# Optimization experiments

Measured on AMD Instinct MI355X. Metric: run time of the kernel, lower is better.

## Reference

```python
import jax, jax.numpy as jnp
import numpy as np

D_MODEL, D_STATE, D_CONV, D_INNER = 1024, 16, 4, 2048
BATCH, SEQ = 4, 2048


def silu(v):
    return v * jax.nn.sigmoid(v)


def setup_inputs() -> dict:
    key = jax.random.key(0)
    ks = jax.random.split(key, 7)
    x = jax.random.normal(ks[0], (BATCH, SEQ, D_MODEL), dtype=jnp.float32)
    s = 0.02
    W_in = jax.random.normal(ks[1], (D_MODEL, 2 * D_INNER), dtype=jnp.float32) * s
    conv_w = jax.random.normal(ks[2], (D_INNER, 1, D_CONV), dtype=jnp.float32) * s  # depthwise (O, I/g=1, K)
    conv_b = jax.random.normal(ks[3], (D_INNER,), dtype=jnp.float32) * s
    W_xproj = jax.random.normal(ks[4], (D_INNER, 2 * D_STATE + 1), dtype=jnp.float32) * s
    A_log = jnp.log(jnp.tile(jnp.arange(1, D_STATE + 1, dtype=jnp.float32), (D_INNER, 1)))
    D = jnp.ones((D_INNER,), dtype=jnp.float32)
    W_out = jax.random.normal(ks[5], (D_INNER, D_MODEL), dtype=jnp.float32) * s
    return {"x": x, "W_in": W_in, "conv_w": conv_w, "conv_b": conv_b,
            "W_xproj": W_xproj, "A_log": A_log, "D": D, "W_out": W_out}


def reference(x, W_in, conv_w, conv_b, W_xproj, A_log, D, W_out):
    B, L, _ = x.shape
    xz = x @ W_in                                   # (B, L, 2*d_inner)
    x_proj, z = jnp.split(xz, 2, axis=-1)
    # Depthwise causal conv: padding=d_conv-1 then truncate to L == left-pad only.
    xc = jax.lax.conv_general_dilated(
        x_proj.transpose(0, 2, 1), conv_w,
        window_strides=(1,), padding=[(D_CONV - 1, 0)],
        feature_group_count=D_INNER,
        dimension_numbers=("NCH", "OIH", "NCH"))
    x_conv = silu((xc + conv_b[None, :, None]).transpose(0, 2, 1))  # (B, L, d_inner)
    ssm = x_conv @ W_xproj                           # (B, L, 1+2*d_state)
    delta = jax.nn.softplus(ssm[..., 0])             # (B, L)
    Bm = ssm[..., 1:1 + D_STATE]                     # (B, L, d_state)
    Cm = ssm[..., 1 + D_STATE:]                      # (B, L, d_state)
    # Original: deltaA = exp(delta*A) and softmax weights are computed but unused.
    deltaB = delta[..., None] * Bm                   # (B, L, d_state)
    # h_approx = mean_L(x outer deltaB): avoid (B,L,d_inner,d_state) intermediate.
    h_mean = jnp.einsum("bld,bln->bdn", x_conv, deltaB) / L  # (B, d_inner, d_state)
    y = jnp.einsum("bdn,bln->bld", h_mean, Cm)       # (B, L, d_inner)
    y = y + D[None, None, :] * x_conv
    y = y * silu(z)
    return y @ W_out                                 # (B, L, d_model)
```

## Files before the change

### kernel.cpp

```cpp
#include <hip/hip_runtime.h>
#include <hip/hip_bf16.h>
#include <stdint.h>

typedef __bf16 bf16x8 __attribute__((ext_vector_type(8)));
typedef float f32x4 __attribute__((ext_vector_type(4)));
typedef float f32x2 __attribute__((ext_vector_type(2)));
typedef unsigned short u16;
typedef u16 ushort4v __attribute__((ext_vector_type(4)));
typedef u16 ushort8v __attribute__((ext_vector_type(8)));

__device__ __forceinline__ u16 f2bf(float f) {
    union { float f; uint32_t u; } v; v.f = f;
    uint32_t u = v.u + 0x7FFFu + ((v.u >> 16) & 1u);
    return (u16)(u >> 16);
}
__device__ __forceinline__ float bf2f(u16 b) {
    union { uint32_t u; float f; } v; v.u = ((uint32_t)b) << 16;
    return v.f;
}
__device__ __forceinline__ float silu_f(float v) {
    return v / (1.0f + __expf(-v));
}
__device__ __forceinline__ void gload_lds16(const u16* g, u16* l) {
    __builtin_amdgcn_global_load_lds(
        (const __attribute__((address_space(1))) void*)g,
        (__attribute__((address_space(3))) void*)l, 16, 0, 0);
}

__device__ __forceinline__ void trans_tile(
        const float* __restrict__ src, u16* __restrict__ dst, int R, int C,
        int bc, int br, float (*tt)[33], int tid) {
    const int tx = tid & 31, ty = tid >> 5;
#pragma unroll
    for (int i = 0; i < 4; i++)
        tt[ty + i * 8][tx] = src[(int64_t)(br * 32 + ty + i * 8) * C + bc * 32 + tx];
    __syncthreads();
#pragma unroll
    for (int i = 0; i < 4; i++)
        dst[(int64_t)(bc * 32 + ty + i * 8) * R + br * 32 + tx] = f2bf(tt[tx][ty + i * 8]);
}

__global__ __launch_bounds__(256) void prep_k(
        const float* __restrict__ x, u16* __restrict__ x_bf,
        const float* __restrict__ Wi, u16* __restrict__ Wti,
        const float* __restrict__ Wo, u16* __restrict__ Wto,
        const float* __restrict__ wx, u16* __restrict__ wxt) {
    __shared__ float tt[32][33];
    const int blk = blockIdx.x, tid = threadIdx.x;
    if (blk < 8192) {
        int i = blk * 256 + tid;
        float4 v = *(const float4*)&x[(int64_t)i * 4];
        ushort4v o = { f2bf(v.x), f2bf(v.y), f2bf(v.z), f2bf(v.w) };
        *(ushort4v*)&x_bf[(int64_t)i * 4] = o;
    } else if (blk < 12288) {
        int t = blk - 8192;
        trans_tile(Wi, Wti, 1024, 4096, t & 127, t >> 7, tt, tid);
    } else if (blk < 14336) {
        int t = blk - 12288;
        trans_tile(Wo, Wto, 2048, 1024, t & 31, t >> 5, tt, tid);
    } else {
        int idx = (blk - 14336) * 256 + tid;
        int j = idx >> 11, d = idx & 2047;
        wxt[idx] = (j < 33) ? f2bf(wx[d * 33 + j]) : (u16)0;
    }
}

template<int M_REP, int WARPS_M, int B_HALVES, bool OUT_BF16>
__global__ __launch_bounds__(512) void gemm_dp(
        const u16* __restrict__ A, const u16* __restrict__ Bt,
        void* __restrict__ Cout, int nbn_sh, int NT, int lda, int ldb, int ldc) {
    constexpr int WARPS_N = 8 / WARPS_M;
    constexpr int QPT = M_REP / 2;
    constexpr int WV_M = M_REP * 16;
    constexpr int BN = WARPS_N * 64;
    constexpr int B_T = BN * 64;

    __shared__ __align__(16) u16 As[2 * 16384];
    __shared__ __align__(16) u16 Bs[2 * B_T];

    const int tid = threadIdx.x;
    const int wave = tid >> 6;
    const int lane = tid & 63;
    const int wm = wave / WARPS_N, wn = wave % WARPS_N;
    const int fr = lane & 15, fq = lane >> 4;

    const int nwg = gridDim.x;
    const int cpx = nwg >> 3;
    const int swz = (blockIdx.x & 7) * cpx + (blockIdx.x >> 3);
    const int bm = swz >> nbn_sh;
    const int bn = swz & ((1 << nbn_sh) - 1);

    const int srow = tid >> 3;
    const int scol8 = ((tid & 7) ^ (srow & 7)) * 8;
    const u16* gA = A + (int64_t)(bm * 256 + srow) * lda + scol8;
    const u16* gB = Bt + (int64_t)(bn * BN + srow) * ldb + scol8;
    const int64_t lda64 = lda, ldb64 = ldb;

    const int ksw0 = ((fq) ^ (fr & 7)) * 8;
    const int ksw1 = ((4 + fq) ^ (fr & 7)) * 8;
    const int arow0 = (wm * WV_M + fr) * 64;
    const int brow0 = (wn * 64 + fr) * 64;

    auto STAGE_A_HALF = [&](int kt, int buf, int h) {
#pragma unroll
        for (int j = 0; j < 2; ++j)
            gload_lds16(gA + (int64_t)(h * 128 + j * 64) * lda64 + kt * 64,
                        &As[buf * 16384 + h * 8192 + j * 4096 + tid * 8]);
    };
    auto STAGE_B_HALF = [&](int kt, int buf, int h) {
#pragma unroll
        for (int j = 0; j < 2; ++j)
            gload_lds16(gB + (int64_t)(h * 128 + j * 64) * ldb64 + kt * 64,
                        &Bs[buf * B_T + h * 8192 + j * 4096 + tid * 8]);
    };

    f32x4 acc[M_REP][4] = {};

    STAGE_A_HALF(0, 0, 0); STAGE_A_HALF(0, 0, 1);
#pragma unroll
    for (int h = 0; h < B_HALVES; ++h) STAGE_B_HALF(0, 0, h);
#pragma unroll
    for (int h = 0; h < B_HALVES; ++h) STAGE_B_HALF(1, 1, h);
    if constexpr (B_HALVES == 2) { asm volatile("s_waitcnt vmcnt(4)" ::: "memory"); }
    else                         { asm volatile("s_waitcnt vmcnt(2)" ::: "memory"); }
    __builtin_amdgcn_s_barrier();

    const int NI = NT >> 1;
    for (int s = 0; s < NI; ++s) {
        const bool more = (s + 1 < NI);
#pragma unroll
        for (int t = 0; t < 2; ++t) {
            const u16* Ab = &As[t * 16384];
            const u16* Bb = &Bs[t * B_T];
            bf16x8 breg[4][2];
            bf16x8 areg[2][2][2];
#pragma unroll
            for (int q = 0; q < QPT; ++q) {
                const int p = q & 1;
                if (q == 0) {
#pragma unroll
                    for (int n = 0; n < 4; ++n) {
                        breg[n][0] = *(const bf16x8*)(Bb + brow0 + n * 1024 + ksw0);
                        breg[n][1] = *(const bf16x8*)(Bb + brow0 + n * 1024 + ksw1);
                    }
#pragma unroll
                    for (int j = 0; j < 2; ++j) {
                        areg[0][j][0] = *(const bf16x8*)(Ab + arow0 + j * 1024 + ksw0);
                        areg[0][j][1] = *(const bf16x8*)(Ab + arow0 + j * 1024 + ksw1);
                    }
                }
                __builtin_amdgcn_s_setprio(1);
                if (q + 1 < QPT) {
#pragma unroll
                    for (int j = 0; j < 2; ++j) {
                        areg[p ^ 1][j][0] = *(const bf16x8*)(Ab + arow0 + (2 * (q + 1) + j) * 1024 + ksw0);
                        areg[p ^ 1][j][1] = *(const bf16x8*)(Ab + arow0 + (2 * (q + 1) + j) * 1024 + ksw1);
                    }
                }
#pragma unroll
                for (int j = 0; j < 2; ++j)
#pragma unroll
                    for (int n = 0; n < 4; ++n) {
                        acc[2 * q + j][n] = __builtin_amdgcn_mfma_f32_16x16x32_bf16(
                            areg[p][j][0], breg[n][0], acc[2 * q + j][n], 0, 0, 0);
                        acc[2 * q + j][n] = __builtin_amdgcn_mfma_f32_16x16x32_bf16(
                            areg[p][j][1], breg[n][1], acc[2 * q + j][n], 0, 0, 0);
                    }
                if (q + 1 < QPT) {
#pragma unroll
                    for (int g = 0; g < 4; ++g) {
                        __builtin_amdgcn_sched_group_barrier(0x008, 2, 0);
                        __builtin_amdgcn_sched_group_barrier(0x100, 1, 0);
                        __builtin_amdgcn_sched_group_barrier(0x008, 2, 0);
                    }
                }
                __builtin_amdgcn_s_setprio(0);
                if constexpr (QPT == 4) {
                    if (t == 0 && q == 0)         STAGE_A_HALF(2 * s + 1, 1, 0);
                    if (t == 0 && q == 1)         STAGE_A_HALF(2 * s + 1, 1, 1);
                    if (t == 0 && q == 2 && more) STAGE_B_HALF(2 * s + 2, 0, 0);
                    if (t == 0 && q == 3 && more) STAGE_B_HALF(2 * s + 2, 0, 1);
                    if (t == 1 && q == 0 && more) STAGE_A_HALF(2 * s + 2, 0, 0);
                    if (t == 1 && q == 1 && more) STAGE_A_HALF(2 * s + 2, 0, 1);
                    if (t == 1 && q == 2 && more) STAGE_B_HALF(2 * s + 3, 1, 0);
                    if (t == 1 && q == 3 && more) STAGE_B_HALF(2 * s + 3, 1, 1);
                } else {
                    if (t == 0 && q == 0)         STAGE_A_HALF(2 * s + 1, 1, 0);
                    if (t == 0 && q == 1) {       STAGE_A_HALF(2 * s + 1, 1, 1);
                        if (more)                 STAGE_B_HALF(2 * s + 2, 0, 0); }
                    if (t == 1 && q == 0 && more) STAGE_A_HALF(2 * s + 2, 0, 0);
                    if (t == 1 && q == 1 && more) { STAGE_A_HALF(2 * s + 2, 0, 1);
                                                    STAGE_B_HALF(2 * s + 3, 1, 0); }
                }
                if (q == QPT - 1) {
                    if (more) {
                        if constexpr (B_HALVES == 2) { asm volatile("s_waitcnt vmcnt(4)" ::: "memory"); }
                        else                         { asm volatile("s_waitcnt vmcnt(2)" ::: "memory"); }
                    } else {
                        asm volatile("s_waitcnt vmcnt(0)" ::: "memory");
                    }
                }
                __builtin_amdgcn_s_barrier();
            }
        }
    }

#pragma unroll
    for (int m = 0; m < M_REP; ++m) {
#pragma unroll
        for (int n = 0; n < 4; ++n) {
            const int col = bn * BN + wn * 64 + n * 16 + fr;
#pragma unroll
            for (int r = 0; r < 4; ++r) {
                const int row = bm * 256 + wm * WV_M + m * 16 + fq * 4 + r;
                if constexpr (OUT_BF16)
                    ((u16*)Cout)[(int64_t)row * ldc + col] = f2bf(acc[m][n][r]);
                else
                    ((float*)Cout)[(int64_t)row * ldc + col] = acc[m][n][r];
            }
        }
    }
}

__global__ __launch_bounds__(256) void conv_ssm_k(
        const u16* __restrict__ xz, const float* __restrict__ cw,
        const float* __restrict__ cb, const u16* __restrict__ wxt,
        u16* __restrict__ xc, float* __restrict__ dB, float* __restrict__ Cm) {
    __shared__ __align__(16) u16 Xs[16][2064];
    __shared__ float Sred[4][16][48];
    __shared__ float deltas[16];
    const int blk = blockIdx.x;
    const int b = blk >> 7, lb = blk & 127;
    const int l0 = lb << 4;
    const int64_t r0 = (int64_t)b * 2048 + l0;
    const int tid = threadIdx.x;
    const int d0 = tid * 8;

    float w[8][4], bias[8];
#pragma unroll
    for (int j = 0; j < 8; j++) {
        float4 wv = *(const float4*)&cw[(d0 + j) * 4];
        w[j][0] = wv.x; w[j][1] = wv.y; w[j][2] = wv.z; w[j][3] = wv.w;
        bias[j] = cb[d0 + j];
    }
    float win[4][8];
#pragma unroll
    for (int r = 0; r < 3; r++) {
        int l = l0 - 3 + r;
        if (l < 0) {
#pragma unroll
            for (int j = 0; j < 8; j++) win[r][j] = 0.f;
        } else {
            ushort8v v = *(const ushort8v*)&xz[((int64_t)b * 2048 + l) * 4096 + d0];
#pragma unroll
            for (int j = 0; j < 8; j++) win[r][j] = bf2f(v[j]);
        }
    }
#pragma unroll
    for (int li = 0; li < 16; li++) {
        ushort8v v = *(const ushort8v*)&xz[(r0 + li) * 4096 + d0];
#pragma unroll
        for (int j = 0; j < 8; j++) win[(3 + li) & 3][j] = bf2f(v[j]);
        ushort8v o;
#pragma unroll
        for (int j = 0; j < 8; j++) {
            float s = bias[j];
#pragma unroll
            for (int k = 0; k < 4; k++) s += w[j][k] * win[(li + k) & 3][j];
            o[j] = f2bf(silu_f(s));
        }
        *(ushort8v*)&xc[(r0 + li) * 2048 + d0] = o;
        *(ushort8v*)&Xs[li][d0] = o;
    }
    __syncthreads();

    const int kc = tid >> 6;
    const int lane = tid & 63;
    const int fr = lane & 15, fq = lane >> 4;
    const u16* bp = wxt + (int64_t)fr * 2048 + kc * 512 + fq * 8;
    const u16* ap = &Xs[fr][kc * 512 + fq * 8];
    f32x4 acc0 = {}, acc1 = {}, acc2 = {};
#pragma unroll 4
    for (int k = 0; k < 512; k += 32) {
        bf16x8 av = *(const bf16x8*)(ap + k);
        bf16x8 b0 = *(const bf16x8*)(bp + k);
        bf16x8 b1 = *(const bf16x8*)(bp + 16 * 2048 + k);
        bf16x8 b2 = *(const bf16x8*)(bp + 32 * 2048 + k);
        acc0 = __builtin_amdgcn_mfma_f32_16x16x32_bf16(av, b0, acc0, 0, 0, 0);
        acc1 = __builtin_amdgcn_mfma_f32_16x16x32_bf16(av, b1, acc1, 0, 0, 0);
        acc2 = __builtin_amdgcn_mfma_f32_16x16x32_bf16(av, b2, acc2, 0, 0, 0);
    }
#pragma unroll
    for (int r = 0; r < 4; r++) {
        Sred[kc][fq * 4 + r][fr]      = acc0[r];
        Sred[kc][fq * 4 + r][16 + fr] = acc1[r];
        Sred[kc][fq * 4 + r][32 + fr] = acc2[r];
    }
    __syncthreads();
    if (tid < 16) {
        float s0 = Sred[0][tid][0] + Sred[1][tid][0] + Sred[2][tid][0] + Sred[3][tid][0];
        deltas[tid] = (s0 > 20.f) ? s0 : log1pf(__expf(s0));
    }
    __syncthreads();
    {
        const int row = tid >> 4, n = tid & 15;
        float sB = Sred[0][row][1 + n] + Sred[1][row][1 + n] +
                   Sred[2][row][1 + n] + Sred[3][row][1 + n];
        float sC = Sred[0][row][17 + n] + Sred[1][row][17 + n] +
                   Sred[2][row][17 + n] + Sred[3][row][17 + n];
        dB[(r0 + row) * 16 + n] = deltas[row] * sB * (1.0f / 2048.0f);
        Cm[(r0 + row) * 16 + n] = sC;
    }
}

__global__ __launch_bounds__(256) void h_part_k(
        const u16* __restrict__ xc, const float* __restrict__ dB,
        float* __restrict__ hp) {
    const int blk = blockIdx.x;
    const int dt = blk & 7, b = (blk >> 3) & 3, lc = blk >> 5;
    const int d = dt * 256 + threadIdx.x;
    const u16* xp = xc + ((int64_t)(b * 2048 + lc * 64)) * 2048 + d;
    const f32x2* dbp = (const f32x2*)(dB + (int64_t)(b * 2048 + lc * 64) * 16);
    f32x2 acc[8] = {};
    for (int l = 0; l < 64; l++) {
        float xv = bf2f(xp[(int64_t)l * 2048]);
#pragma unroll
        for (int q = 0; q < 8; q++) acc[q] += dbp[l * 8 + q] * xv;
    }
    float* o = hp + ((int64_t)((lc * 4 + b) * 2048 + d)) * 16;
#pragma unroll
    for (int q = 0; q < 8; q++) *(f32x2*)&o[q * 2] = acc[q];
}

__global__ void h_red_k(const float* __restrict__ hp, float* __restrict__ h) {
    const int i = blockIdx.x * 256 + threadIdx.x;
    float s = 0.f;
#pragma unroll
    for (int c = 0; c < 32; c++) s += hp[(int64_t)c * 131072 + i];
    h[i] = s;
}

__global__ __launch_bounds__(256) void y_gate_k(
        u16* __restrict__ xz, const u16* __restrict__ xc,
        const float* __restrict__ h, const float* __restrict__ Cm,
        const float* __restrict__ Dp) {
    const int blk = blockIdx.x;
    const int lc = blk & 63, dt = (blk >> 6) & 1, b = blk >> 7;
    const int d0 = dt * 1024 + threadIdx.x * 4;
    const float* hpp = h + ((int64_t)(b * 2048 + d0)) * 16;
    float hreg[4][16];
#pragma unroll
    for (int i = 0; i < 4; i++)
#pragma unroll
        for (int n = 0; n < 16; n++) hreg[i][n] = hpp[i * 16 + n];
    float Dv[4];
#pragma unroll
    for (int i = 0; i < 4; i++) Dv[i] = Dp[d0 + i];
    __shared__ float Cs[32][16];
    if (threadIdx.x < 128)
        ((float4*)&Cs[0][0])[threadIdx.x] =
            ((const float4*)(Cm + (int64_t)(b * 2048 + lc * 32) * 16))[threadIdx.x];
    __syncthreads();
    for (int li = 0; li < 32; li++) {
        const int64_t rowz = (int64_t)(b * 2048 + lc * 32 + li);
        ushort4v xcv = *(const ushort4v*)&xc[rowz * 2048 + d0];
        ushort4v zv = *(const ushort4v*)&xz[rowz * 4096 + 2048 + d0];
        ushort4v o;
#pragma unroll
        for (int i = 0; i < 4; i++) {
            float s = Dv[i] * bf2f(xcv[i]);
#pragma unroll
            for (int n = 0; n < 16; n++) s += hreg[i][n] * Cs[li][n];
            o[i] = f2bf(s * silu_f(bf2f(zv[i])));
        }
        *(ushort4v*)&xz[rowz * 4096 + d0] = o;
    }
}

extern "C" void kernel_launch(void* const* d_in, const int* in_sizes, int n_in,
                              void* d_out, int out_size, void* d_ws, size_t ws_size,
                              hipStream_t stream) {
    (void)in_sizes; (void)n_in; (void)out_size; (void)ws_size;
    const float* x      = (const float*)d_in[0];
    const float* W_in   = (const float*)d_in[1];
    const float* conv_w = (const float*)d_in[2];
    const float* conv_b = (const float*)d_in[3];
    const float* W_xp   = (const float*)d_in[4];
    const float* Dp     = (const float*)d_in[6];
    const float* W_out  = (const float*)d_in[7];
    float* out = (float*)d_out;
    char* ws = (char*)d_ws;

    u16*   x_bf   = (u16*)(ws);
    float* dB     = (float*)(ws);
    float* Cm     = (float*)(ws + 524288);
    float* h      = (float*)(ws + 1048576);
    float* hp     = (float*)(ws + 1572864);
    u16*   Wt_in  = (u16*)(ws + 16777216);
    u16*   Wt_out = (u16*)(ws + 25165824);
    u16*   Wxt    = (u16*)(ws + 29360128);
    u16*   xz     = (u16*)(ws + 29556736);
    u16*   xcv    = (u16*)(ws + 96665600);

    prep_k<<<14720, 256, 0, stream>>>(x, x_bf, W_in, Wt_in, W_out, Wt_out, W_xp, Wxt);
    gemm_dp<8, 2, 2, true><<<512, 512, 0, stream>>>(x_bf, Wt_in, xz, 4, 16, 1024, 1024, 4096);
    conv_ssm_k<<<512, 256, 0, stream>>>(xz, conv_w, conv_b, Wxt, xcv, dB, Cm);
    h_part_k<<<1024, 256, 0, stream>>>(xcv, dB, hp);
    h_red_k<<<512, 256, 0, stream>>>(hp, h);
    y_gate_k<<<512, 256, 0, stream>>>(xz, xcv, h, Cm, Dp);
    gemm_dp<4, 4, 1, false><<<256, 512, 0, stream>>>(xz, Wt_out, out, 3, 32, 4096, 2048, 1024);
}
```

Before: 209.8 us.

## Triple-buffer A tiles in GEMM and lengthen h_part chunks to cut reduction

The GEMM's A operand moves from double to triple buffering in LDS, with rotating slot indices. This lets A for tile k+2 be prefetched while tiles k and k+1 are consumed, and the vmcnt waits are raised to allow more loads in flight. Separately, h_part_k now processes 256-row chunks instead of 64, so it launches 4x fewer blocks and h_red_k sums 8 partials instead of 32. The trade-offs are more LDS per GEMM block (possibly lower occupancy) and less parallelism in h_part_k.

New measurement: 223.3 us. 6.4% more time.

```diff
diff --git a/kernel.cpp b/kernel.cpp
--- a/kernel.cpp
+++ b/kernel.cpp
@@ -75,7 +75,7 @@
     constexpr int BN = WARPS_N * 64;
     constexpr int B_T = BN * 64;
 
-    __shared__ __align__(16) u16 As[2 * 16384];
+    __shared__ __align__(16) u16 As[3 * 16384];
     __shared__ __align__(16) u16 Bs[2 * B_T];
 
     const int tid = threadIdx.x;
@@ -101,11 +101,11 @@
     const int arow0 = (wm * WV_M + fr) * 64;
     const int brow0 = (wn * 64 + fr) * 64;
 
-    auto STAGE_A_HALF = [&](int kt, int buf, int h) {
+    auto STAGE_A_HALF = [&](int kt, int slot, int h) {
 #pragma unroll
         for (int j = 0; j < 2; ++j)
             gload_lds16(gA + (int64_t)(h * 128 + j * 64) * lda64 + kt * 64,
-                        &As[buf * 16384 + h * 8192 + j * 4096 + tid * 8]);
+                        &As[slot * 16384 + h * 8192 + j * 4096 + tid * 8]);
     };
     auto STAGE_B_HALF = [&](int kt, int buf, int h) {
 #pragma unroll
@@ -119,18 +119,21 @@
     STAGE_A_HALF(0, 0, 0); STAGE_A_HALF(0, 0, 1);
 #pragma unroll
     for (int h = 0; h < B_HALVES; ++h) STAGE_B_HALF(0, 0, h);
+    STAGE_A_HALF(1, 1, 0); STAGE_A_HALF(1, 1, 1);
 #pragma unroll
     for (int h = 0; h < B_HALVES; ++h) STAGE_B_HALF(1, 1, h);
-    if constexpr (B_HALVES == 2) { asm volatile("s_waitcnt vmcnt(4)" ::: "memory"); }
-    else                         { asm volatile("s_waitcnt vmcnt(2)" ::: "memory"); }
+    if constexpr (B_HALVES == 2) { asm volatile("s_waitcnt vmcnt(8)" ::: "memory"); }
+    else                         { asm volatile("s_waitcnt vmcnt(6)" ::: "memory"); }
     __builtin_amdgcn_s_barrier();
 
+    int a0 = 0, a1 = 1, a2 = 2;
     const int NI = NT >> 1;
     for (int s = 0; s < NI; ++s) {
         const bool more = (s + 1 < NI);
 #pragma unroll
         for (int t = 0; t < 2; ++t) {
-            const u16* Ab = &As[t * 16384];
+            const int aslot = (t == 0) ? a0 : a1;
+            const u16* Ab = &As[aslot * 16384];
             const u16* Bb = &Bs[t * B_T];
             bf16x8 breg[4][2];
             bf16x8 areg[2][2][2];
@@ -175,27 +178,22 @@
                     }
                 }
                 __builtin_amdgcn_s_setprio(0);
+                const int ktn = 2 * s + 2 + t;
+                const int asl = (t == 0) ? a2 : a0;
                 if constexpr (QPT == 4) {
-                    if (t == 0 && q == 0)         STAGE_A_HALF(2 * s + 1, 1, 0);
-                    if (t == 0 && q == 1)         STAGE_A_HALF(2 * s + 1, 1, 1);
-                    if (t == 0 && q == 2 && more) STAGE_B_HALF(2 * s + 2, 0, 0);
-                    if (t == 0 && q == 3 && more) STAGE_B_HALF(2 * s + 2, 0, 1);
-                    if (t == 1 && q == 0 && more) STAGE_A_HALF(2 * s + 2, 0, 0);
-                    if (t == 1 && q == 1 && more) STAGE_A_HALF(2 * s + 2, 0, 1);
-                    if (t == 1 && q == 2 && more) STAGE_B_HALF(2 * s + 3, 1, 0);
-                    if (t == 1 && q == 3 && more) STAGE_B_HALF(2 * s + 3, 1, 1);
+                    if (q == 0 && more) STAGE_A_HALF(ktn, asl, 0);
+                    if (q == 1 && more) STAGE_A_HALF(ktn, asl, 1);
+                    if (q == 2 && more) STAGE_B_HALF(ktn, t, 0);
+                    if (q == 3 && more) STAGE_B_HALF(ktn, t, 1);
                 } else {
-                    if (t == 0 && q == 0)         STAGE_A_HALF(2 * s + 1, 1, 0);
-                    if (t == 0 && q == 1) {       STAGE_A_HALF(2 * s + 1, 1, 1);
-                        if (more)                 STAGE_B_HALF(2 * s + 2, 0, 0); }
-                    if (t == 1 && q == 0 && more) STAGE_A_HALF(2 * s + 2, 0, 0);
-                    if (t == 1 && q == 1 && more) { STAGE_A_HALF(2 * s + 2, 0, 1);
-                                                    STAGE_B_HALF(2 * s + 3, 1, 0); }
+                    if (q == 0 && more) STAGE_A_HALF(ktn, asl, 0);
+                    if (q == 1 && more) { STAGE_A_HALF(ktn, asl, 1);
+                                          STAGE_B_HALF(ktn, t, 0); }
                 }
                 if (q == QPT - 1) {
                     if (more) {
-                        if constexpr (B_HALVES == 2) { asm volatile("s_waitcnt vmcnt(4)" ::: "memory"); }
-                        else                         { asm volatile("s_waitcnt vmcnt(2)" ::: "memory"); }
+                        if constexpr (B_HALVES == 2) { asm volatile("s_waitcnt vmcnt(8)" ::: "memory"); }
+                        else                         { asm volatile("s_waitcnt vmcnt(6)" ::: "memory"); }
                     } else {
                         asm volatile("s_waitcnt vmcnt(0)" ::: "memory");
                     }
@@ -203,6 +201,7 @@
                 __builtin_amdgcn_s_barrier();
             }
         }
+        int tmp = a0; a0 = a2; a2 = a1; a1 = tmp;
     }
 
 #pragma unroll
@@ -319,10 +318,10 @@
     const int blk = blockIdx.x;
     const int dt = blk & 7, b = (blk >> 3) & 3, lc = blk >> 5;
     const int d = dt * 256 + threadIdx.x;
-    const u16* xp = xc + ((int64_t)(b * 2048 + lc * 64)) * 2048 + d;
-    const f32x2* dbp = (const f32x2*)(dB + (int64_t)(b * 2048 + lc * 64) * 16);
+    const u16* xp = xc + ((int64_t)(b * 2048 + lc * 256)) * 2048 + d;
+    const f32x2* dbp = (const f32x2*)(dB + (int64_t)(b * 2048 + lc * 256) * 16);
     f32x2 acc[8] = {};
-    for (int l = 0; l < 64; l++) {
+    for (int l = 0; l < 256; l++) {
         float xv = bf2f(xp[(int64_t)l * 2048]);
 #pragma unroll
         for (int q = 0; q < 8; q++) acc[q] += dbp[l * 8 + q] * xv;
@@ -336,7 +335,7 @@
     const int i = blockIdx.x * 256 + threadIdx.x;
     float s = 0.f;
 #pragma unroll
-    for (int c = 0; c < 32; c++) s += hp[(int64_t)c * 131072 + i];
+    for (int c = 0; c < 8; c++) s += hp[(int64_t)c * 131072 + i];
     h[i] = s;
 }
 
@@ -405,7 +404,7 @@
     prep_k<<<14720, 256, 0, stream>>>(x, x_bf, W_in, Wt_in, W_out, Wt_out, W_xp, Wxt);
     gemm_dp<8, 2, 2, true><<<512, 512, 0, stream>>>(x_bf, Wt_in, xz, 4, 16, 1024, 1024, 4096);
     conv_ssm_k<<<512, 256, 0, stream>>>(xz, conv_w, conv_b, Wxt, xcv, dB, Cm);
-    h_part_k<<<1024, 256, 0, stream>>>(xcv, dB, hp);
+    h_part_k<<<256, 256, 0, stream>>>(xcv, dB, hp);
     h_red_k<<<512, 256, 0, stream>>>(hp, h);
     y_gate_k<<<512, 256, 0, stream>>>(xz, xcv, h, Cm, Dp);
     gemm_dp<4, 4, 1, false><<<256, 512, 0, stream>>>(xz, Wt_out, out, 3, 32, 4096, 2048, 1024);
```
